# Kernel tuning notes

Measured on AMD Instinct MI355X. Metric: run time of the kernel, lower is better.

## Reference

```python
import jax, jax.numpy as jnp
import numpy as np
import math

B, A, I, O = 4096, 32, 256, 256


def setup_inputs() -> dict:
    key = jax.random.key(0)
    kx, kw, kb = jax.random.split(key, 3)
    x = jax.random.normal(kx, (B, A, I), dtype=jnp.float32)
    # kaiming_uniform_(a=sqrt(5)) on [A, O, I]: fan_in = I, bound = sqrt(6/((1+5)*I)) = 1/sqrt(I)
    wb = 1.0 / math.sqrt(I)
    weight = jax.random.uniform(kw, (A, O, I), minval=-wb, maxval=wb, dtype=jnp.float32)
    bb = 1.0 / math.sqrt(I)
    bias = jax.random.uniform(kb, (A, O), minval=-bb, maxval=bb, dtype=jnp.float32)
    return {"x": x, "weight": weight, "bias": bias}


def reference(x, weight, bias):
    # per-assignment batched GEMM: weight [A,O,I], x [B,A,I] -> [B,A,O]
    return jnp.einsum('aoi,bai->bao', weight, x) + bias
```

## Files before the change

kernel.cpp:

```cpp
#include <hip/hip_runtime.h>

typedef __attribute__((ext_vector_type(4))) float f32x4;
typedef __attribute__((ext_vector_type(2))) unsigned u32x2;
typedef __attribute__((ext_vector_type(8))) short bf16x8;

constexpr int Bsz = 4096, Asz = 32, Isz = 256, Osz = 256;
constexpr int NI = 16;

__device__ inline unsigned cvtpk(float lo, float hi) {
    unsigned r;
    asm("v_cvt_pk_bf16_f32 %0, %1, %2" : "=v"(r) : "v"(lo), "v"(hi));
    return r;
}

__global__ __launch_bounds__(512, 2) void al_gemm(const float* __restrict__ x,
                                                  const float* __restrict__ wsrc,
                                                  const float* __restrict__ bias,
                                                  float* __restrict__ out)
{
    __shared__ char sA[2][16384];
    __shared__ char sB[131072];

    const int p  = blockIdx.x;
    const int a  = (p & 7) * 4 + ((p >> 3) & 3);
    const int b0 = (p >> 5) * 512;

    const int t    = threadIdx.x;
    const int w    = t >> 6;
    const int lane = t & 63;
    const int llo  = lane & 15, lhi = lane >> 4;

    const float* fs[4];
    int wadr[4];
#pragma unroll
    for (int j = 0; j < 4; ++j) {
        const int lr = 4 * w + j;
        fs[j]   = x + ((size_t)(b0 + lr) * Asz + a) * Isz + lane * 4;
        wadr[j] = lr * 512 + (((lane >> 1) ^ lr) << 4) + (lane & 1) * 8;
    }

    f32x4 L[4];
#pragma unroll
    for (int j = 0; j < 4; ++j) L[j] = *(const f32x4*)fs[j];
    asm volatile("" : "+v"(L[0]), "+v"(L[1]), "+v"(L[2]), "+v"(L[3]));

    {
        const float* wa = wsrc + (size_t)a * (Osz * Isz);
#pragma unroll
        for (int i = 0; i < 16; ++i) {
            const int s     = i * 512 + t;
            const int o     = s >> 5;
            const int kt    = (s >> 2) & 7;
            const int nf    = s >> 9;
            const int lane_ = (o & 15) | ((s & 3) << 4);
            f32x4 lo = *(const f32x4*)(wa + (size_t)s * 8);
            f32x4 hi = *(const f32x4*)(wa + (size_t)s * 8 + 4);
            union { bf16x8 v; unsigned u[4]; } r;
            r.u[0] = cvtpk(lo[0], lo[1]); r.u[1] = cvtpk(lo[2], lo[3]);
            r.u[2] = cvtpk(hi[0], hi[1]); r.u[3] = cvtpk(hi[2], hi[3]);
            *(bf16x8*)&sB[(((kt * 16 + nf) * 64) + lane_) * 16] = r.v;
        }
    }

    const float bv0 = bias[a * Osz + w * 32 + llo];
    const float bv1 = bias[a * Osz + w * 32 + 16 + llo];

#pragma unroll
    for (int j = 0; j < 4; ++j)
        *(u32x2*)&sA[0][wadr[j]] = (u32x2){cvtpk(L[j][0], L[j][1]), cvtpk(L[j][2], L[j][3])};

    __syncthreads();

    const int lr1 = llo + 16;

    for (int tn = 0; tn < NI; ++tn) {
        if (tn < NI - 1) {
            const size_t o_ = (size_t)(tn + 1) * (32 * Asz * Isz);
#pragma unroll
            for (int j = 0; j < 4; ++j) L[j] = *(const f32x4*)(fs[j] + o_);
            asm volatile("" : "+v"(L[0]), "+v"(L[1]), "+v"(L[2]), "+v"(L[3]));
        }

        const char* As = &sA[tn & 1][0];
        f32x4 acc00 = (f32x4)(bv0), acc01 = (f32x4)(bv1);
        f32x4 acc10 = (f32x4)(bv0), acc11 = (f32x4)(bv1);
        __builtin_amdgcn_s_setprio(1);
#pragma unroll
        for (int kt = 0; kt < 8; ++kt) {
            const int c = kt * 4 + lhi;
            const bf16x8 aF0 = *(const bf16x8*)&As[llo * 512 + ((c ^ llo) << 4)];
            const bf16x8 aF1 = *(const bf16x8*)&As[lr1 * 512 + ((c ^ lr1) << 4)];
            const bf16x8 bF0 = *(const bf16x8*)&sB[(kt * 16 + 2 * w) * 1024 + lane * 16];
            const bf16x8 bF1 = *(const bf16x8*)&sB[(kt * 16 + 2 * w + 1) * 1024 + lane * 16];
            acc00 = __builtin_amdgcn_mfma_f32_16x16x32_bf16(aF0, bF0, acc00, 0, 0, 0);
            acc01 = __builtin_amdgcn_mfma_f32_16x16x32_bf16(aF0, bF1, acc01, 0, 0, 0);
            acc10 = __builtin_amdgcn_mfma_f32_16x16x32_bf16(aF1, bF0, acc10, 0, 0, 0);
            acc11 = __builtin_amdgcn_mfma_f32_16x16x32_bf16(aF1, bF1, acc11, 0, 0, 0);
        }
        __builtin_amdgcn_s_setprio(0);

        const int trow = b0 + tn * 32 + lhi * 4;
        float* op0 = out + ((size_t)trow * Asz + a) * Osz + w * 32 + llo;
        float* op1 = op0 + (size_t)16 * Asz * Osz;
#pragma unroll
        for (int r2 = 0; r2 < 4; ++r2) {
            op0[(size_t)r2 * Asz * Osz]      = acc00[r2];
            op0[(size_t)r2 * Asz * Osz + 16] = acc01[r2];
            op1[(size_t)r2 * Asz * Osz]      = acc10[r2];
            op1[(size_t)r2 * Asz * Osz + 16] = acc11[r2];
        }

        if (tn < NI - 1) {
            char* Ad = &sA[(tn + 1) & 1][0];
#pragma unroll
            for (int j = 0; j < 4; ++j)
                *(u32x2*)&Ad[wadr[j]] = (u32x2){cvtpk(L[j][0], L[j][1]), cvtpk(L[j][2], L[j][3])};
        }

        __syncthreads();
    }
}

extern "C" void kernel_launch(void* const* d_in, const int* in_sizes, int n_in,
                              void* d_out, int out_size, void* d_ws, size_t ws_size,
                              hipStream_t stream) {
    const float* x    = (const float*)d_in[0];
    const float* w    = (const float*)d_in[1];
    const float* bias = (const float*)d_in[2];
    float* out        = (float*)d_out;
    al_gemm<<<dim3(256), dim3(512), 0, stream>>>(x, w, bias, out);
}
```

Measured before the change: 58.79 us.

## Process 64-row x tiles per iteration with single LDS buffer

Each iteration now covers 64 batch rows instead of 32, so there are half as many iterations and each B fragment read from LDS is reused across four M sub-tiles. The double-buffered 16KB A tiles become a single 32KB tile. Each thread loads eight contiguous float4s per row segment and writes 16-byte packed bf16 stores with a new XOR swizzle. The tile is written to LDS at the top of each iteration behind an explicit waitcnt and barrier, so conversion and storing no longer overlap the previous tile's MFMAs, and register pressure rises with eight accumulators and eight prefetch vectors.

```diff
diff --git a/kernel.cpp b/kernel.cpp
--- a/kernel.cpp
+++ b/kernel.cpp
@@ -1,11 +1,11 @@
 #include <hip/hip_runtime.h>
 
 typedef __attribute__((ext_vector_type(4))) float f32x4;
-typedef __attribute__((ext_vector_type(2))) unsigned u32x2;
+typedef __attribute__((ext_vector_type(4))) unsigned u32x4;
 typedef __attribute__((ext_vector_type(8))) short bf16x8;
 
-constexpr int Bsz = 4096, Asz = 32, Isz = 256, Osz = 256;
-constexpr int NI = 16;
+constexpr int Asz = 32, Isz = 256, Osz = 256;
+constexpr int NI = 8;
 
 __device__ inline unsigned cvtpk(float lo, float hi) {
     unsigned r;
@@ -18,7 +18,7 @@
                                                   const float* __restrict__ bias,
                                                   float* __restrict__ out)
 {
-    __shared__ char sA[2][16384];
+    __shared__ char sA[32768];
     __shared__ char sB[131072];
 
     const int p  = blockIdx.x;
@@ -30,19 +30,19 @@
     const int lane = t & 63;
     const int llo  = lane & 15, lhi = lane >> 4;
 
-    const float* fs[4];
+    const int lr = 8 * w + (lane >> 3);
+    const int c0 = (lane & 7) * 4;
+    const float* xrow = x + ((size_t)(b0 + lr) * Asz + a) * Isz + (lane & 7) * 32;
     int wadr[4];
 #pragma unroll
-    for (int j = 0; j < 4; ++j) {
-        const int lr = 4 * w + j;
-        fs[j]   = x + ((size_t)(b0 + lr) * Asz + a) * Isz + lane * 4;
-        wadr[j] = lr * 512 + (((lane >> 1) ^ lr) << 4) + (lane & 1) * 8;
-    }
+    for (int j = 0; j < 4; ++j)
+        wadr[j] = lr * 512 + (((c0 + j) ^ (lr & 31)) << 4);
 
-    f32x4 L[4];
+    f32x4 L[8];
 #pragma unroll
-    for (int j = 0; j < 4; ++j) L[j] = *(const f32x4*)fs[j];
-    asm volatile("" : "+v"(L[0]), "+v"(L[1]), "+v"(L[2]), "+v"(L[3]));
+    for (int j = 0; j < 8; ++j) L[j] = *(const f32x4*)(xrow + j * 4);
+    asm volatile("" : "+v"(L[0]), "+v"(L[1]), "+v"(L[2]), "+v"(L[3]),
+                      "+v"(L[4]), "+v"(L[5]), "+v"(L[6]), "+v"(L[7]));
 
     {
         const float* wa = wsrc + (size_t)a * (Osz * Isz);
@@ -65,59 +65,59 @@
     const float bv0 = bias[a * Osz + w * 32 + llo];
     const float bv1 = bias[a * Osz + w * 32 + 16 + llo];
 
+    for (int i = 0; i < NI; ++i) {
 #pragma unroll
-    for (int j = 0; j < 4; ++j)
-        *(u32x2*)&sA[0][wadr[j]] = (u32x2){cvtpk(L[j][0], L[j][1]), cvtpk(L[j][2], L[j][3])};
+        for (int j = 0; j < 4; ++j) {
+            u32x4 pk;
+            pk[0] = cvtpk(L[2*j][0],   L[2*j][1]);
+            pk[1] = cvtpk(L[2*j][2],   L[2*j][3]);
+            pk[2] = cvtpk(L[2*j+1][0], L[2*j+1][1]);
+            pk[3] = cvtpk(L[2*j+1][2], L[2*j+1][3]);
+            *(u32x4*)&sA[wadr[j]] = pk;
+        }
+        asm volatile("s_waitcnt lgkmcnt(0)" ::: "memory");
+        __builtin_amdgcn_s_barrier();
 
-    __syncthreads();
-
-    const int lr1 = llo + 16;
-
-    for (int tn = 0; tn < NI; ++tn) {
-        if (tn < NI - 1) {
-            const size_t o_ = (size_t)(tn + 1) * (32 * Asz * Isz);
+        if (i < NI - 1) {
+            const float* nx = xrow + (size_t)(i + 1) * (64 * Asz * Isz);
 #pragma unroll
-            for (int j = 0; j < 4; ++j) L[j] = *(const f32x4*)(fs[j] + o_);
-            asm volatile("" : "+v"(L[0]), "+v"(L[1]), "+v"(L[2]), "+v"(L[3]));
+            for (int j = 0; j < 8; ++j) L[j] = *(const f32x4*)(nx + j * 4);
+            asm volatile("" : "+v"(L[0]), "+v"(L[1]), "+v"(L[2]), "+v"(L[3]),
+                              "+v"(L[4]), "+v"(L[5]), "+v"(L[6]), "+v"(L[7]));
         }
 
-        const char* As = &sA[tn & 1][0];
-        f32x4 acc00 = (f32x4)(bv0), acc01 = (f32x4)(bv1);
-        f32x4 acc10 = (f32x4)(bv0), acc11 = (f32x4)(bv1);
+        f32x4 acc[4][2];
+#pragma unroll
+        for (int m = 0; m < 4; ++m) { acc[m][0] = (f32x4)(bv0); acc[m][1] = (f32x4)(bv1); }
+
         __builtin_amdgcn_s_setprio(1);
 #pragma unroll
         for (int kt = 0; kt < 8; ++kt) {
             const int c = kt * 4 + lhi;
-            const bf16x8 aF0 = *(const bf16x8*)&As[llo * 512 + ((c ^ llo) << 4)];
-            const bf16x8 aF1 = *(const bf16x8*)&As[lr1 * 512 + ((c ^ lr1) << 4)];
             const bf16x8 bF0 = *(const bf16x8*)&sB[(kt * 16 + 2 * w) * 1024 + lane * 16];
             const bf16x8 bF1 = *(const bf16x8*)&sB[(kt * 16 + 2 * w + 1) * 1024 + lane * 16];
-            acc00 = __builtin_amdgcn_mfma_f32_16x16x32_bf16(aF0, bF0, acc00, 0, 0, 0);
-            acc01 = __builtin_amdgcn_mfma_f32_16x16x32_bf16(aF0, bF1, acc01, 0, 0, 0);
-            acc10 = __builtin_amdgcn_mfma_f32_16x16x32_bf16(aF1, bF0, acc10, 0, 0, 0);
-            acc11 = __builtin_amdgcn_mfma_f32_16x16x32_bf16(aF1, bF1, acc11, 0, 0, 0);
+#pragma unroll
+            for (int m = 0; m < 4; ++m) {
+                const int row = m * 16 + llo;
+                const bf16x8 aF = *(const bf16x8*)&sA[row * 512 + ((c ^ (row & 31)) << 4)];
+                acc[m][0] = __builtin_amdgcn_mfma_f32_16x16x32_bf16(aF, bF0, acc[m][0], 0, 0, 0);
+                acc[m][1] = __builtin_amdgcn_mfma_f32_16x16x32_bf16(aF, bF1, acc[m][1], 0, 0, 0);
+            }
         }
         __builtin_amdgcn_s_setprio(0);
 
-        const int trow = b0 + tn * 32 + lhi * 4;
-        float* op0 = out + ((size_t)trow * Asz + a) * Osz + w * 32 + llo;
-        float* op1 = op0 + (size_t)16 * Asz * Osz;
 #pragma unroll
-        for (int r2 = 0; r2 < 4; ++r2) {
-            op0[(size_t)r2 * Asz * Osz]      = acc00[r2];
-            op0[(size_t)r2 * Asz * Osz + 16] = acc01[r2];
-            op1[(size_t)r2 * Asz * Osz]      = acc10[r2];
-            op1[(size_t)r2 * Asz * Osz + 16] = acc11[r2];
+        for (int m = 0; m < 4; ++m) {
+            const int trow = b0 + i * 64 + m * 16 + lhi * 4;
+            float* op = out + ((size_t)trow * Asz + a) * Osz + w * 32 + llo;
+#pragma unroll
+            for (int r2 = 0; r2 < 4; ++r2) {
+                op[(size_t)r2 * Asz * Osz]      = acc[m][0][r2];
+                op[(size_t)r2 * Asz * Osz + 16] = acc[m][1][r2];
+            }
         }
 
-        if (tn < NI - 1) {
-            char* Ad = &sA[(tn + 1) & 1][0];
-#pragma unroll
-            for (int j = 0; j < 4; ++j)
-                *(u32x2*)&Ad[wadr[j]] = (u32x2){cvtpk(L[j][0], L[j][1]), cvtpk(L[j][2], L[j][3])};
-        }
-
-        __syncthreads();
+        __builtin_amdgcn_s_barrier();
     }
 }
 
```

Result: slower. 63.70 us (+8.3%).
